# Optimization experiments

Measured on AMD Instinct MI355X. Metric: run time of the kernel, lower is better.

Reference implementation:

```python
import jax, jax.numpy as jnp
import numpy as np

HEADS = 16
NEG = -1.0e9


def setup_inputs() -> dict:
    key = jax.random.key(0)
    ks = jax.random.split(key, 6)
    B, T, E = 4, 2048, 1024
    s = 1.0 / np.sqrt(E)
    x = jax.random.normal(ks[0], (B, T, E), dtype=jnp.float32)
    Wq = jax.random.normal(ks[1], (E, E), dtype=jnp.float32) * s
    Wk = jax.random.normal(ks[2], (E, E), dtype=jnp.float32) * s
    Wv = jax.random.normal(ks[3], (E, E), dtype=jnp.float32) * s
    Wout = jax.random.normal(ks[4], (E, E), dtype=jnp.float32) * s
    bout = jax.random.normal(ks[5], (E,), dtype=jnp.float32) * 0.01
    return {"x": x, "Wq": Wq, "Wk": Wk, "Wv": Wv, "Wout": Wout, "bout": bout}


def reference(x, Wq, Wk, Wv, Wout, bout):
    B, T, E = x.shape
    H = HEADS
    D = E // H
    # nn.Linear(bias=False): y = x @ W.T
    Q = (x @ Wq.T).reshape(B, T, H, D).transpose(0, 2, 1, 3)  # [B,H,T,D]
    K = (x @ Wk.T).reshape(B, T, H, D).transpose(0, 2, 1, 3)
    V = (x @ Wv.T).reshape(B, T, H, D).transpose(0, 2, 1, 3)
    scores = jnp.einsum('bhqd,bhkd->bhqk', Q, K) / jnp.sqrt(jnp.float32(D))
    causal = jnp.tril(jnp.ones((T, T), dtype=bool))  # [T,T]
    scores = jnp.where(causal[None, None, :, :], scores, NEG)
    attn = jax.nn.softmax(scores, axis=-1)
    ctx = jnp.einsum('bhqk,bhkd->bhqd', attn, V)
    ctx = ctx.transpose(0, 2, 1, 3).reshape(B, T, E)
    return ctx @ Wout.T + bout
```

## Files before the change

### kernel.cpp

```cpp
#include <hip/hip_runtime.h>
#include <hip/hip_bf16.h>
#include <stdint.h>
#include <math.h>

#define B_ 4
#define T_ 2048
#define E_ 1024
#define H_ 16
#define D_ 64

typedef __attribute__((ext_vector_type(8))) short short8;
typedef __attribute__((ext_vector_type(4))) short short4v;
typedef __attribute__((ext_vector_type(4))) float f32x4;

#define MFMA_BF16(a, b, c) __builtin_amdgcn_mfma_f32_16x16x32_bf16((a), (b), (c), 0, 0, 0)

__device__ __forceinline__ unsigned short f2bf(float f) {
  union { float f; unsigned u; } v; v.f = f;
  unsigned r = v.u + 0x7FFFu + ((v.u >> 16) & 1u);
  return (unsigned short)(r >> 16);
}

#define GLOAD_LDS16(g, l)                                                        \
  __builtin_amdgcn_global_load_lds((const __attribute__((address_space(1))) void*)(g), \
                                   (__attribute__((address_space(3))) void*)(l), 16, 0, 0)

__global__ __launch_bounds__(256) void cvt_all(const float* __restrict__ x,
                                               const float* __restrict__ w0,
                                               const float* __restrict__ w1,
                                               const float* __restrict__ w2,
                                               const float* __restrict__ w3,
                                               unsigned short* __restrict__ xb,
                                               unsigned short* __restrict__ wb) {
  const int NX8 = 1048576;
  int i = blockIdx.x * blockDim.x + threadIdx.x;
  const float* src;
  unsigned short* dst;
  size_t off;
  if (i < NX8) {
    src = x; dst = xb; off = (size_t)i * 8;
  } else {
    int j = i - NX8;
    int which = j >> 17;
    int o = j & 131071;
    src = (which == 0) ? w0 : (which == 1) ? w1 : (which == 2) ? w2 : w3;
    dst = wb + ((size_t)which << 20);
    off = (size_t)o * 8;
  }
  const float4* p = (const float4*)(src + off);
  float4 a = p[0], b = p[1];
  short8 r;
  r[0] = (short)f2bf(a.x); r[1] = (short)f2bf(a.y);
  r[2] = (short)f2bf(a.z); r[3] = (short)f2bf(a.w);
  r[4] = (short)f2bf(b.x); r[5] = (short)f2bf(b.y);
  r[6] = (short)f2bf(b.z); r[7] = (short)f2bf(b.w);
  *(short8*)(dst + off) = r;
}


#define GEMM2_BODY(A_PTR, B_PTR)                                                  \
  const int K = E_;                                                               \
  const int NT = 16;                                                              \
  const int tid = threadIdx.x;                                                    \
  const int wid = tid >> 6;                                                       \
  const int lane = tid & 63;                                                      \
  const int lr = lane & 15;                                                       \
  const int lk = lane >> 4;                                                       \
  const int wm = wid >> 2, wn = wid & 3;                                          \
  const int srow = lane >> 3;                                                     \
  const int scol = ((lane & 7) ^ srow) * 8;                                       \
  const int rswz = (lr & 7) << 4;                                                 \
  const int kofs0 = (lk * 16) ^ rswz;                                             \
  const int kofs1 = (64 + lk * 16) ^ rswz;                                        \
  f32x4 acc[4][4] = {};                                                           \
  short8 af[4][2], bf0[2][2], bf1[2][2];                                          \
  auto stageA = [&](int tau) {                                                    \
    char* dst = lds + (tau & 1) * 49152 + wid * 1024;                             \
    const unsigned short* src = (A_PTR) + (size_t)(m0 + wid * 8 + srow) * K +     \
                                tau * 64 + scol;                                  \
    GLOAD_LDS16(src, dst);                                                        \
    GLOAD_LDS16(src + (size_t)64 * K, dst + 8192);                                \
  };                                                                              \
  auto stageB = [&](int tau) {                                                    \
    char* dst = lds + (tau & 1) * 49152 + 16384 + wid * 1024;                     \
    const unsigned short* src = (B_PTR) + (size_t)(n0 + wid * 8 + srow) * K +     \
                                tau * 64 + scol;                                  \
    GLOAD_LDS16(src, dst);                                                        \
    GLOAD_LDS16(src + (size_t)64 * K, dst + 8192);                                \
    GLOAD_LDS16(src + (size_t)128 * K, dst + 16384);                              \
    GLOAD_LDS16(src + (size_t)192 * K, dst + 24576);                              \
  };                                                                              \
  stageB(0); stageA(0); stageB(1);                                                \
  asm volatile("s_waitcnt vmcnt(4)" ::: "memory");                                \
  __builtin_amdgcn_s_barrier();                                                   \
  for (int t = 0; t < NT; ++t) {                                                  \
    char* bufA = lds + (t & 1) * 49152;                                           \
    char* bufB = bufA + 16384;                                                    \
    _Pragma("unroll")                                                             \
    for (int i = 0; i < 4; ++i) {                                                 \
      int row = wm * 64 + i * 16 + lr;                                            \
      af[i][0] = *(const short8*)(bufA + row * 128 + kofs0);                      \
      af[i][1] = *(const short8*)(bufA + row * 128 + kofs1);                      \
    }                                                                             \
    _Pragma("unroll")                                                             \
    for (int i = 0; i < 2; ++i) {                                                 \
      int row0 = wn * 64 + i * 16 + lr;                                           \
      int row1 = wn * 64 + (2 + i) * 16 + lr;                                     \
      bf0[i][0] = *(const short8*)(bufB + row0 * 128 + kofs0);                    \
      bf0[i][1] = *(const short8*)(bufB + row0 * 128 + kofs1);                    \
      bf1[i][0] = *(const short8*)(bufB + row1 * 128 + kofs0);                    \
      bf1[i][1] = *(const short8*)(bufB + row1 * 128 + kofs1);                    \
    }                                                                             \
    if (t + 1 < NT) stageA(t + 1);                                                \
    __builtin_amdgcn_s_barrier();                                                 \
    asm volatile("s_waitcnt lgkmcnt(0)" ::: "memory");                            \
    __builtin_amdgcn_sched_barrier(0);                                            \
    __builtin_amdgcn_s_setprio(1);                                                \
    _Pragma("unroll")                                                             \
    for (int i = 0; i < 4; ++i)                                                   \
      _Pragma("unroll")                                                           \
      for (int jn = 0; jn < 2; ++jn) {                                            \
        acc[i][jn] = MFMA_BF16(af[i][0], bf0[jn][0], acc[i][jn]);                 \
        acc[i][jn] = MFMA_BF16(af[i][1], bf0[jn][1], acc[i][jn]);                 \
      }                                                                           \
    __builtin_amdgcn_s_setprio(0);                                                \
    __builtin_amdgcn_s_barrier();                                                 \
    if (t + 2 < NT) stageB(t + 2);                                                \
    __builtin_amdgcn_s_setprio(1);                                                \
    _Pragma("unroll")                                                             \
    for (int i = 0; i < 4; ++i)                                                   \
      _Pragma("unroll")                                                           \
      for (int jn = 0; jn < 2; ++jn) {                                            \
        acc[i][2 + jn] = MFMA_BF16(af[i][0], bf1[jn][0], acc[i][2 + jn]);         \
        acc[i][2 + jn] = MFMA_BF16(af[i][1], bf1[jn][1], acc[i][2 + jn]);         \
      }                                                                           \
    __builtin_amdgcn_s_setprio(0);                                                \
    if (t < NT - 2) asm volatile("s_waitcnt vmcnt(4)" ::: "memory");              \
    else            asm volatile("s_waitcnt vmcnt(0)" ::: "memory");              \
    __builtin_amdgcn_s_barrier();                                                 \
  }

__global__ __launch_bounds__(512) void gemm_qkv2(const unsigned short* __restrict__ A,
                                                 const unsigned short* __restrict__ Wq,
                                                 const unsigned short* __restrict__ Wk,
                                                 const unsigned short* __restrict__ Wv,
                                                 unsigned short* __restrict__ Qo,
                                                 unsigned short* __restrict__ Ko,
                                                 unsigned short* __restrict__ Vo) {
  __shared__ __align__(16) char lds[98304];
  const int bid = blockIdx.x;
  const int xcd = bid & 7;
  const int p = bid >> 3;
  const int m0 = (xcd * 8 + (p & 7)) * 128;
  const int j = p >> 3;
  const int n0 = (j & 3) * 256;
  const int sel = j >> 2;
  const unsigned short* Bm = (sel == 0) ? Wq : (sel == 1) ? Wk : Wv;

  GEMM2_BODY(A, Bm)

  unsigned short* outp = (sel == 0) ? Qo : (sel == 1) ? Ko : Vo;
#pragma unroll
  for (int mi = 0; mi < 4; ++mi)
#pragma unroll
    for (int ni = 0; ni < 4; ++ni) {
      int row0 = m0 + wm * 64 + mi * 16 + lk * 4;
      int col = n0 + wn * 64 + ni * 16 + lr;
      int b = row0 >> 11, t0 = row0 & (T_ - 1), h = col >> 6, d = col & (D_ - 1);
      if (sel == 2) {
        short4v vv;
#pragma unroll
        for (int r = 0; r < 4; ++r) vv[r] = (short)f2bf(acc[mi][ni][r]);
        *(short4v*)&outp[(((size_t)(b * H_ + h)) * D_ + d) * T_ + t0] = vv;
      } else {
#pragma unroll
        for (int r = 0; r < 4; ++r)
          outp[(((size_t)(b * H_ + h)) * T_ + t0 + r) * D_ + d] = f2bf(acc[mi][ni][r]);
      }
    }
}

__global__ __launch_bounds__(512) void gemm_out2(const unsigned short* __restrict__ A,
                                                 const unsigned short* __restrict__ Wout,
                                                 float* __restrict__ outp,
                                                 const float* __restrict__ bias) {
  __shared__ __align__(16) char lds[98304];
  const int bid = blockIdx.x;
  const int xcd = bid & 7;
  const int p = bid >> 3;
  const int m0 = (xcd * 8 + (p & 7)) * 128;
  const int n0 = (p >> 3) * 256;

  GEMM2_BODY(A, Wout)

#pragma unroll
  for (int mi = 0; mi < 4; ++mi)
#pragma unroll
    for (int ni = 0; ni < 4; ++ni) {
      int row0 = m0 + wm * 64 + mi * 16 + lk * 4;
      int col = n0 + wn * 64 + ni * 16 + lr;
      float bv = bias[col];
#pragma unroll
      for (int r = 0; r < 4; ++r)
        outp[(size_t)(row0 + r) * E_ + col] = acc[mi][ni][r] + bv;
    }
}

__global__ __launch_bounds__(64) void attn_fused(const unsigned short* __restrict__ Q,
                                                 const unsigned short* __restrict__ K,
                                                 const unsigned short* __restrict__ VT,
                                                 unsigned short* __restrict__ ctx) {
  __shared__ __align__(16) unsigned short Pl[2][64 * 72];
  const int lane = threadIdx.x & 63;
  const int lr = lane & 15;
  const int lk = lane >> 4;

  const int bid = blockIdx.x;
  const int xcd = bid & 7;
  const int p = bid >> 3;
  const int bh = xcd * 8 + (p & 7);
  const int c = 31 - (p >> 3);
  const int q0 = c * 64;

  const unsigned short* Qh = Q + (size_t)bh * T_ * D_;
  const unsigned short* Kh = K + (size_t)bh * T_ * D_;
  const unsigned short* Vh = VT + (size_t)bh * T_ * D_;
  char* bufA = (char*)&Pl[0][0];
  char* bufB = (char*)&Pl[1][0];

  const float SC = 0.125f * 1.44269504089f;

  short8 vones;
#pragma unroll
  for (int j = 0; j < 8; ++j) vones[j] = (short)0x3F80;

  short8 qfA[2][2], qfB[2][2];
#pragma unroll
  for (int a = 0; a < 2; ++a)
#pragma unroll
    for (int kb = 0; kb < 2; ++kb) {
      qfA[a][kb] = *(const short8*)&Qh[(size_t)(q0 + a * 16 + lr) * D_ + kb * 32 + lk * 8];
      qfB[a][kb] = *(const short8*)&Qh[(size_t)(q0 + 32 + a * 16 + lr) * D_ + kb * 32 + lk * 8];
    }

  f32x4 oA[2][4] = {}, oB[2][4] = {};
  f32x4 lsA[2] = {}, lsB[2] = {};
  float mA[2] = {-1e30f, -1e30f}, mB[2] = {-1e30f, -1e30f};

  const int nt = c + 1;

  auto loadK = [&](short8(&kf)[2][4], int t) {
    const unsigned short* Kt = Kh + (size_t)t * 64 * D_;
#pragma unroll
    for (int kb = 0; kb < 2; ++kb)
#pragma unroll
      for (int n = 0; n < 4; ++n)
        kf[kb][n] = *(const short8*)&Kt[(size_t)(n * 16 + lr) * D_ + kb * 32 + lk * 8];
  };
  auto loadV = [&](short8(&v)[2][4], int t) {
    const unsigned short* Vtt = Vh + (size_t)t * 64;
#pragma unroll
    for (int kb = 0; kb < 2; ++kb)
#pragma unroll
      for (int nd = 0; nd < 4; ++nd)
        v[kb][nd] = *(const short8*)&Vtt[(size_t)(nd * 16 + lr) * T_ + kb * 32 + lk * 8];
  };
  auto rowmax = [&](f32x4(&st)[2][4], float(&pm)[2]) {
#pragma unroll
    for (int a = 0; a < 2; ++a) {
      float m0 = fmaxf(fmaxf(st[a][0][0], st[a][1][0]), fmaxf(st[a][2][0], st[a][3][0]));
      float m1 = fmaxf(fmaxf(st[a][0][1], st[a][1][1]), fmaxf(st[a][2][1], st[a][3][1]));
      float m2 = fmaxf(fmaxf(st[a][0][2], st[a][1][2]), fmaxf(st[a][2][2], st[a][3][2]));
      float m3 = fmaxf(fmaxf(st[a][0][3], st[a][1][3]), fmaxf(st[a][2][3], st[a][3][3]));
      float mx = fmaxf(fmaxf(m0, m1), fmaxf(m2, m3));
      mx = fmaxf(mx, __shfl_xor(mx, 16));
      mx = fmaxf(mx, __shfl_xor(mx, 32));
      pm[a] = mx * SC;
    }
  };
  auto rescale1 = [&](float(&pm)[2], float(&mrun)[2], f32x4(&ls)[2], f32x4(&o)[2][4]) {
#pragma unroll
    for (int a = 0; a < 2; ++a) {
      float mnew = fmaxf(mrun[a], pm[a]);
      float sc = exp2f(mrun[a] - mnew);
      mrun[a] = mnew;
#pragma unroll
      for (int r = 0; r < 4; ++r) {
        float sco = __shfl(sc, (lane & 48) | (lk * 4 + r));
        ls[a][r] *= sco;
#pragma unroll
        for (int nd = 0; nd < 4; ++nd) o[a][nd][r] *= sco;
      }
    }
  };
  auto pack = [&](f32x4(&st)[2][4], float(&mrun)[2], char* buf, int rb) {
#pragma unroll
    for (int a = 0; a < 2; ++a)
#pragma unroll
      for (int n = 0; n < 4; ++n) {
        float2 p01, p23;
        p01.x = exp2f(fmaf(st[a][n][0], SC, -mrun[a]));
        p01.y = exp2f(fmaf(st[a][n][1], SC, -mrun[a]));
        p23.x = exp2f(fmaf(st[a][n][2], SC, -mrun[a]));
        p23.y = exp2f(fmaf(st[a][n][3], SC, -mrun[a]));
        __hip_bfloat162 b01 = __float22bfloat162_rn(p01);
        __hip_bfloat162 b23 = __float22bfloat162_rn(p23);
        uint2 w;
        w.x = *(unsigned*)&b01;
        w.y = *(unsigned*)&b23;
        *(uint2*)(buf + (rb + a * 16 + lr) * 144 + n * 32 + lk * 8) = w;
      }
  };
  auto pv = [&](char* buf, short8(&v)[2][4]) {
#pragma unroll
    for (int kb = 0; kb < 2; ++kb) {
      short8 pfA0 = *(const short8*)(buf + (0 + lr) * 144 + kb * 64 + lk * 16);
      short8 pfA1 = *(const short8*)(buf + (16 + lr) * 144 + kb * 64 + lk * 16);
      short8 pfB0 = *(const short8*)(buf + (32 + lr) * 144 + kb * 64 + lk * 16);
      short8 pfB1 = *(const short8*)(buf + (48 + lr) * 144 + kb * 64 + lk * 16);
#pragma unroll
      for (int nd = 0; nd < 4; ++nd) {
        oA[0][nd] = MFMA_BF16(pfA0, v[kb][nd], oA[0][nd]);
        oA[1][nd] = MFMA_BF16(pfA1, v[kb][nd], oA[1][nd]);
        oB[0][nd] = MFMA_BF16(pfB0, v[kb][nd], oB[0][nd]);
        oB[1][nd] = MFMA_BF16(pfB1, v[kb][nd], oB[1][nd]);
      }
      lsA[0] = MFMA_BF16(pfA0, vones, lsA[0]);
      lsA[1] = MFMA_BF16(pfA1, vones, lsA[1]);
      lsB[0] = MFMA_BF16(pfB0, vones, lsB[0]);
      lsB[1] = MFMA_BF16(pfB1, vones, lsB[1]);
    }
  };

  auto tile = [&](int i, bool diag, bool doPV,
                  short8(&kfc)[2][4], short8(&kfn)[2][4],
                  short8(&vp)[2][4], short8(&vc)[2][4],
                  char* bufp, char* bufc, int tnext) {
    loadK(kfn, tnext);
    loadV(vc, i);
    f32x4 stA[2][4] = {}, stB[2][4] = {};
#pragma unroll
    for (int kb = 0; kb < 2; ++kb)
#pragma unroll
      for (int a = 0; a < 2; ++a)
#pragma unroll
        for (int n = 0; n < 4; ++n) {
          stA[a][n] = MFMA_BF16(kfc[kb][n], qfA[a][kb], stA[a][n]);
          stB[a][n] = MFMA_BF16(kfc[kb][n], qfB[a][kb], stB[a][n]);
        }
    if (diag) {
#pragma unroll
      for (int a = 0; a < 2; ++a)
#pragma unroll
        for (int n = 0; n < 4; ++n)
#pragma unroll
          for (int r = 0; r < 4; ++r) {
            if (n * 16 + lk * 4 + r > 0 + a * 16 + lr) stA[a][n][r] = -3e38f;
            if (n * 16 + lk * 4 + r > 32 + a * 16 + lr) stB[a][n][r] = -3e38f;
          }
    }
    float pmA[2], pmB[2];
    rowmax(stA, pmA);
    rowmax(stB, pmB);
    float need = fmaxf(fmaxf(pmA[0] - mA[0], pmA[1] - mA[1]),
                       fmaxf(pmB[0] - mB[0], pmB[1] - mB[1]));
    if (doPV) pv(bufp, vp);
    if (__any(need > 8.f)) {
      rescale1(pmA, mA, lsA, oA);
      rescale1(pmB, mB, lsB, oB);
    }
    pack(stA, mA, bufc, 0);
    pack(stB, mB, bufc, 32);
  };

  short8 kf0[2][4], kf1[2][4], v0[2][4], v1[2][4];

  loadK(kf0, 0);
  tile(0, nt == 1, false, kf0, kf1, v1, v0, bufB, bufA, (1 < nt) ? 1 : 0);

  int i = 1;
  while (i < nt) {
    tile(i, i == nt - 1, true, kf1, kf0, v0, v1, bufA, bufB, (i + 1 < nt) ? i + 1 : i);
    if (++i >= nt) break;
    tile(i, i == nt - 1, true, kf0, kf1, v1, v0, bufB, bufA, (i + 1 < nt) ? i + 1 : i);
    ++i;
  }
  if ((nt - 1) & 1) pv(bufB, v1);
  else              pv(bufA, v0);

  const int b = bh >> 4, h2 = bh & 15;
#pragma unroll
  for (int a = 0; a < 2; ++a)
#pragma unroll
    for (int r = 0; r < 4; ++r) {
      float invA = 1.0f / lsA[a][r];
      float invB = 1.0f / lsB[a][r];
      int tA = q0 + a * 16 + lk * 4 + r;
      int tB = tA + 32;
#pragma unroll
      for (int nd = 0; nd < 4; ++nd) {
        ctx[((size_t)b * T_ + tA) * E_ + h2 * D_ + nd * 16 + lr] = f2bf(oA[a][nd][r] * invA);
        ctx[((size_t)b * T_ + tB) * E_ + h2 * D_ + nd * 16 + lr] = f2bf(oB[a][nd][r] * invB);
      }
    }
}

extern "C" void kernel_launch(void* const* d_in, const int* in_sizes, int n_in,
                              void* d_out, int out_size, void* d_ws, size_t ws_size,
                              hipStream_t stream) {
  const float* x    = (const float*)d_in[0];
  const float* Wq   = (const float*)d_in[1];
  const float* Wk   = (const float*)d_in[2];
  const float* Wv   = (const float*)d_in[3];
  const float* Wout = (const float*)d_in[4];
  const float* bout = (const float*)d_in[5];
  float* out = (float*)d_out;

  const size_t MT = (size_t)B_ * T_;
  const size_t XE = MT * E_;
  const size_t WE = (size_t)E_ * E_;

  size_t need = (XE * 5 + WE * 4) * sizeof(unsigned short);
  if (ws_size < need) return;

  unsigned short* xb  = (unsigned short*)d_ws;
  unsigned short* wqb = xb + XE;
  unsigned short* wkb = wqb + WE;
  unsigned short* wvb = wkb + WE;
  unsigned short* wob = wvb + WE;
  unsigned short* Qb  = wob + WE;
  unsigned short* Kb  = Qb + XE;
  unsigned short* VTb = Kb + XE;
  unsigned short* ctx = VTb + XE;

  cvt_all<<<6144, 256, 0, stream>>>(x, Wq, Wk, Wv, Wout, xb, wqb);

  gemm_qkv2<<<768, 512, 0, stream>>>(xb, wqb, wkb, wvb, Qb, Kb, VTb);

  attn_fused<<<2048, 64, 0, stream>>>(Qb, Kb, VTb, ctx);

  gemm_out2<<<256, 512, 0, stream>>>(ctx, wob, out, bout);
}
```

Baseline: 167.2 us.

## Share K/V tiles via LDS across 8 waves per 256-row query block

The attention kernel changes from one 64-thread wave per 64-query chunk, which read K and V straight from global memory into registers, to 512-thread blocks. Each block covers 256 queries, with each wave owning 32 rows. K and V tiles are staged cooperatively into double-buffered, swizzled LDS with global_load_lds, so one copy serves all eight waves and global and L2 traffic drop. The cost is a block-wide barrier every tile, and waves whose causal range ends early sit idle while their siblings finish. The register-level software pipelining that overlapped PV with the next QK is also gone, and per-wave MFMA work per tile is halved.

Measured after the change: 169.2 us. No clear change (+1.2%).

```diff
diff --git a/kernel.cpp b/kernel.cpp
--- a/kernel.cpp
+++ b/kernel.cpp
@@ -56,7 +56,6 @@
   r[6] = (short)f2bf(b.z); r[7] = (short)f2bf(b.w);
   *(short8*)(dst + off) = r;
 }
-
 
 #define GEMM2_BODY(A_PTR, B_PTR)                                                  \
   const int K = E_;                                                               \
@@ -206,12 +205,15 @@
     }
 }
 
-__global__ __launch_bounds__(64) void attn_fused(const unsigned short* __restrict__ Q,
-                                                 const unsigned short* __restrict__ K,
-                                                 const unsigned short* __restrict__ VT,
-                                                 unsigned short* __restrict__ ctx) {
-  __shared__ __align__(16) unsigned short Pl[2][64 * 72];
-  const int lane = threadIdx.x & 63;
+__global__ __launch_bounds__(512) void attn_fused8(const unsigned short* __restrict__ Q,
+                                                   const unsigned short* __restrict__ K,
+                                                   const unsigned short* __restrict__ VT,
+                                                   unsigned short* __restrict__ ctx) {
+  __shared__ __align__(16) char kvb[2][16384];
+  __shared__ __align__(16) char Pl[8][4608];
+  const int tid = threadIdx.x;
+  const int wid = tid >> 6;
+  const int lane = tid & 63;
   const int lr = lane & 15;
   const int lk = lane >> 4;
 
@@ -219,189 +221,163 @@
   const int xcd = bid & 7;
   const int p = bid >> 3;
   const int bh = xcd * 8 + (p & 7);
-  const int c = 31 - (p >> 3);
-  const int q0 = c * 64;
+  const int Qb = 7 - (p >> 3);
 
   const unsigned short* Qh = Q + (size_t)bh * T_ * D_;
   const unsigned short* Kh = K + (size_t)bh * T_ * D_;
   const unsigned short* Vh = VT + (size_t)bh * T_ * D_;
-  char* bufA = (char*)&Pl[0][0];
-  char* bufB = (char*)&Pl[1][0];
+  char* Pb = Pl[wid];
+
+  const int q0w = Qb * 256 + wid * 32;
+  const int diag = q0w >> 6;
+  const int ql0 = (wid & 1) * 32;
+  const int NTb = 4 * Qb + 4;
 
   const float SC = 0.125f * 1.44269504089f;
 
+  const int srow = tid >> 3;
+  const int scol = ((tid & 7) ^ (srow & 7)) * 8;
+  const int rswz = (lr & 7) << 4;
+
+  auto stage = [&](int t) {
+    char* dst = kvb[t & 1] + tid * 16;
+    GLOAD_LDS16(Kh + (size_t)(t * 64 + srow) * D_ + scol, dst);
+    GLOAD_LDS16(Vh + (size_t)srow * T_ + t * 64 + scol, dst + 8192);
+  };
+
   short8 vones;
 #pragma unroll
   for (int j = 0; j < 8; ++j) vones[j] = (short)0x3F80;
 
-  short8 qfA[2][2], qfB[2][2];
+  short8 qf[2][2];
 #pragma unroll
   for (int a = 0; a < 2; ++a)
 #pragma unroll
-    for (int kb = 0; kb < 2; ++kb) {
-      qfA[a][kb] = *(const short8*)&Qh[(size_t)(q0 + a * 16 + lr) * D_ + kb * 32 + lk * 8];
-      qfB[a][kb] = *(const short8*)&Qh[(size_t)(q0 + 32 + a * 16 + lr) * D_ + kb * 32 + lk * 8];
-    }
-
-  f32x4 oA[2][4] = {}, oB[2][4] = {};
-  f32x4 lsA[2] = {}, lsB[2] = {};
-  float mA[2] = {-1e30f, -1e30f}, mB[2] = {-1e30f, -1e30f};
-
-  const int nt = c + 1;
-
-  auto loadK = [&](short8(&kf)[2][4], int t) {
-    const unsigned short* Kt = Kh + (size_t)t * 64 * D_;
-#pragma unroll
     for (int kb = 0; kb < 2; ++kb)
-#pragma unroll
-      for (int n = 0; n < 4; ++n)
-        kf[kb][n] = *(const short8*)&Kt[(size_t)(n * 16 + lr) * D_ + kb * 32 + lk * 8];
-  };
-  auto loadV = [&](short8(&v)[2][4], int t) {
-    const unsigned short* Vtt = Vh + (size_t)t * 64;
-#pragma unroll
-    for (int kb = 0; kb < 2; ++kb)
-#pragma unroll
-      for (int nd = 0; nd < 4; ++nd)
-        v[kb][nd] = *(const short8*)&Vtt[(size_t)(nd * 16 + lr) * T_ + kb * 32 + lk * 8];
-  };
-  auto rowmax = [&](f32x4(&st)[2][4], float(&pm)[2]) {
-#pragma unroll
-    for (int a = 0; a < 2; ++a) {
-      float m0 = fmaxf(fmaxf(st[a][0][0], st[a][1][0]), fmaxf(st[a][2][0], st[a][3][0]));
-      float m1 = fmaxf(fmaxf(st[a][0][1], st[a][1][1]), fmaxf(st[a][2][1], st[a][3][1]));
-      float m2 = fmaxf(fmaxf(st[a][0][2], st[a][1][2]), fmaxf(st[a][2][2], st[a][3][2]));
-      float m3 = fmaxf(fmaxf(st[a][0][3], st[a][1][3]), fmaxf(st[a][2][3], st[a][3][3]));
-      float mx = fmaxf(fmaxf(m0, m1), fmaxf(m2, m3));
-      mx = fmaxf(mx, __shfl_xor(mx, 16));
-      mx = fmaxf(mx, __shfl_xor(mx, 32));
-      pm[a] = mx * SC;
-    }
-  };
-  auto rescale1 = [&](float(&pm)[2], float(&mrun)[2], f32x4(&ls)[2], f32x4(&o)[2][4]) {
-#pragma unroll
-    for (int a = 0; a < 2; ++a) {
-      float mnew = fmaxf(mrun[a], pm[a]);
-      float sc = exp2f(mrun[a] - mnew);
-      mrun[a] = mnew;
-#pragma unroll
-      for (int r = 0; r < 4; ++r) {
-        float sco = __shfl(sc, (lane & 48) | (lk * 4 + r));
-        ls[a][r] *= sco;
-#pragma unroll
-        for (int nd = 0; nd < 4; ++nd) o[a][nd][r] *= sco;
+      qf[a][kb] = *(const short8*)&Qh[(size_t)(q0w + a * 16 + lr) * D_ + kb * 32 + lk * 8];
+
+  f32x4 o[2][4] = {};
+  f32x4 lsum[2] = {};
+  float mrun[2] = {-1e30f, -1e30f};
+
+  stage(0);
+  asm volatile("s_waitcnt vmcnt(0)" ::: "memory");
+  __builtin_amdgcn_s_barrier();
+
+  for (int t = 0; t < NTb; ++t) {
+    if (t + 1 < NTb) stage(t + 1);
+
+    if (t <= diag) {
+      char* kb_ = kvb[t & 1];
+      char* vb_ = kvb[t & 1] + 8192;
+
+      short8 kf[2][4];
+#pragma unroll
+      for (int kb = 0; kb < 2; ++kb)
+#pragma unroll
+        for (int n = 0; n < 4; ++n)
+          kf[kb][n] = *(const short8*)(kb_ + (n * 16 + lr) * 128 + ((kb * 64 + lk * 16) ^ rswz));
+
+      f32x4 st[2][4] = {};
+#pragma unroll
+      for (int kb = 0; kb < 2; ++kb)
+#pragma unroll
+        for (int a = 0; a < 2; ++a)
+#pragma unroll
+          for (int n = 0; n < 4; ++n)
+            st[a][n] = MFMA_BF16(kf[kb][n], qf[a][kb], st[a][n]);
+
+      if (t == diag) {
+#pragma unroll
+        for (int a = 0; a < 2; ++a)
+#pragma unroll
+          for (int n = 0; n < 4; ++n)
+#pragma unroll
+            for (int r = 0; r < 4; ++r)
+              if (n * 16 + lk * 4 + r > ql0 + a * 16 + lr) st[a][n][r] = -3e38f;
+      }
+
+      float pm[2];
+#pragma unroll
+      for (int a = 0; a < 2; ++a) {
+        float m0 = fmaxf(fmaxf(st[a][0][0], st[a][1][0]), fmaxf(st[a][2][0], st[a][3][0]));
+        float m1 = fmaxf(fmaxf(st[a][0][1], st[a][1][1]), fmaxf(st[a][2][1], st[a][3][1]));
+        float m2 = fmaxf(fmaxf(st[a][0][2], st[a][1][2]), fmaxf(st[a][2][2], st[a][3][2]));
+        float m3 = fmaxf(fmaxf(st[a][0][3], st[a][1][3]), fmaxf(st[a][2][3], st[a][3][3]));
+        float mx = fmaxf(fmaxf(m0, m1), fmaxf(m2, m3));
+        mx = fmaxf(mx, __shfl_xor(mx, 16));
+        mx = fmaxf(mx, __shfl_xor(mx, 32));
+        pm[a] = mx * SC;
+      }
+      float need = fmaxf(pm[0] - mrun[0], pm[1] - mrun[1]);
+
+      if (__any(need > 8.f)) {
+#pragma unroll
+        for (int a = 0; a < 2; ++a) {
+          float mnew = fmaxf(mrun[a], pm[a]);
+          float sc = exp2f(mrun[a] - mnew);
+          mrun[a] = mnew;
+#pragma unroll
+          for (int r = 0; r < 4; ++r) {
+            float sco = __shfl(sc, (lane & 48) | (lk * 4 + r));
+            lsum[a][r] *= sco;
+#pragma unroll
+            for (int nd = 0; nd < 4; ++nd) o[a][nd][r] *= sco;
+          }
+        }
+      }
+
+#pragma unroll
+      for (int a = 0; a < 2; ++a)
+#pragma unroll
+        for (int n = 0; n < 4; ++n) {
+          float2 p01, p23;
+          p01.x = exp2f(fmaf(st[a][n][0], SC, -mrun[a]));
+          p01.y = exp2f(fmaf(st[a][n][1], SC, -mrun[a]));
+          p23.x = exp2f(fmaf(st[a][n][2], SC, -mrun[a]));
+          p23.y = exp2f(fmaf(st[a][n][3], SC, -mrun[a]));
+          __hip_bfloat162 b01 = __float22bfloat162_rn(p01);
+          __hip_bfloat162 b23 = __float22bfloat162_rn(p23);
+          uint2 w;
+          w.x = *(unsigned*)&b01;
+          w.y = *(unsigned*)&b23;
+          *(uint2*)(Pb + (a * 16 + lr) * 144 + n * 32 + lk * 8) = w;
+        }
+
+      short8 vf[2][4];
+#pragma unroll
+      for (int kb = 0; kb < 2; ++kb)
+#pragma unroll
+        for (int nd = 0; nd < 4; ++nd)
+          vf[kb][nd] = *(const short8*)(vb_ + (nd * 16 + lr) * 128 + ((kb * 64 + lk * 16) ^ rswz));
+#pragma unroll
+      for (int kb = 0; kb < 2; ++kb) {
+        short8 pf0 = *(const short8*)(Pb + (0 + lr) * 144 + kb * 64 + lk * 16);
+        short8 pf1 = *(const short8*)(Pb + (16 + lr) * 144 + kb * 64 + lk * 16);
+#pragma unroll
+        for (int nd = 0; nd < 4; ++nd) {
+          o[0][nd] = MFMA_BF16(pf0, vf[kb][nd], o[0][nd]);
+          o[1][nd] = MFMA_BF16(pf1, vf[kb][nd], o[1][nd]);
+        }
+        lsum[0] = MFMA_BF16(pf0, vones, lsum[0]);
+        lsum[1] = MFMA_BF16(pf1, vones, lsum[1]);
       }
     }
-  };
-  auto pack = [&](f32x4(&st)[2][4], float(&mrun)[2], char* buf, int rb) {
-#pragma unroll
-    for (int a = 0; a < 2; ++a)
-#pragma unroll
-      for (int n = 0; n < 4; ++n) {
-        float2 p01, p23;
-        p01.x = exp2f(fmaf(st[a][n][0], SC, -mrun[a]));
-        p01.y = exp2f(fmaf(st[a][n][1], SC, -mrun[a]));
-        p23.x = exp2f(fmaf(st[a][n][2], SC, -mrun[a]));
-        p23.y = exp2f(fmaf(st[a][n][3], SC, -mrun[a]));
-        __hip_bfloat162 b01 = __float22bfloat162_rn(p01);
-        __hip_bfloat162 b23 = __float22bfloat162_rn(p23);
-        uint2 w;
-        w.x = *(unsigned*)&b01;
-        w.y = *(unsigned*)&b23;
-        *(uint2*)(buf + (rb + a * 16 + lr) * 144 + n * 32 + lk * 8) = w;
-      }
-  };
-  auto pv = [&](char* buf, short8(&v)[2][4]) {
-#pragma unroll
-    for (int kb = 0; kb < 2; ++kb) {
-      short8 pfA0 = *(const short8*)(buf + (0 + lr) * 144 + kb * 64 + lk * 16);
-      short8 pfA1 = *(const short8*)(buf + (16 + lr) * 144 + kb * 64 + lk * 16);
-      short8 pfB0 = *(const short8*)(buf + (32 + lr) * 144 + kb * 64 + lk * 16);
-      short8 pfB1 = *(const short8*)(buf + (48 + lr) * 144 + kb * 64 + lk * 16);
-#pragma unroll
-      for (int nd = 0; nd < 4; ++nd) {
-        oA[0][nd] = MFMA_BF16(pfA0, v[kb][nd], oA[0][nd]);
-        oA[1][nd] = MFMA_BF16(pfA1, v[kb][nd], oA[1][nd]);
-        oB[0][nd] = MFMA_BF16(pfB0, v[kb][nd], oB[0][nd]);
-        oB[1][nd] = MFMA_BF16(pfB1, v[kb][nd], oB[1][nd]);
-      }
-      lsA[0] = MFMA_BF16(pfA0, vones, lsA[0]);
-      lsA[1] = MFMA_BF16(pfA1, vones, lsA[1]);
-      lsB[0] = MFMA_BF16(pfB0, vones, lsB[0]);
-      lsB[1] = MFMA_BF16(pfB1, vones, lsB[1]);
-    }
-  };
-
-  auto tile = [&](int i, bool diag, bool doPV,
-                  short8(&kfc)[2][4], short8(&kfn)[2][4],
-                  short8(&vp)[2][4], short8(&vc)[2][4],
-                  char* bufp, char* bufc, int tnext) {
-    loadK(kfn, tnext);
-    loadV(vc, i);
-    f32x4 stA[2][4] = {}, stB[2][4] = {};
-#pragma unroll
-    for (int kb = 0; kb < 2; ++kb)
-#pragma unroll
-      for (int a = 0; a < 2; ++a)
-#pragma unroll
-        for (int n = 0; n < 4; ++n) {
-          stA[a][n] = MFMA_BF16(kfc[kb][n], qfA[a][kb], stA[a][n]);
-          stB[a][n] = MFMA_BF16(kfc[kb][n], qfB[a][kb], stB[a][n]);
-        }
-    if (diag) {
-#pragma unroll
-      for (int a = 0; a < 2; ++a)
-#pragma unroll
-        for (int n = 0; n < 4; ++n)
-#pragma unroll
-          for (int r = 0; r < 4; ++r) {
-            if (n * 16 + lk * 4 + r > 0 + a * 16 + lr) stA[a][n][r] = -3e38f;
-            if (n * 16 + lk * 4 + r > 32 + a * 16 + lr) stB[a][n][r] = -3e38f;
-          }
-    }
-    float pmA[2], pmB[2];
-    rowmax(stA, pmA);
-    rowmax(stB, pmB);
-    float need = fmaxf(fmaxf(pmA[0] - mA[0], pmA[1] - mA[1]),
-                       fmaxf(pmB[0] - mB[0], pmB[1] - mB[1]));
-    if (doPV) pv(bufp, vp);
-    if (__any(need > 8.f)) {
-      rescale1(pmA, mA, lsA, oA);
-      rescale1(pmB, mB, lsB, oB);
-    }
-    pack(stA, mA, bufc, 0);
-    pack(stB, mB, bufc, 32);
-  };
-
-  short8 kf0[2][4], kf1[2][4], v0[2][4], v1[2][4];
-
-  loadK(kf0, 0);
-  tile(0, nt == 1, false, kf0, kf1, v1, v0, bufB, bufA, (1 < nt) ? 1 : 0);
-
-  int i = 1;
-  while (i < nt) {
-    tile(i, i == nt - 1, true, kf1, kf0, v0, v1, bufA, bufB, (i + 1 < nt) ? i + 1 : i);
-    if (++i >= nt) break;
-    tile(i, i == nt - 1, true, kf0, kf1, v1, v0, bufB, bufA, (i + 1 < nt) ? i + 1 : i);
-    ++i;
+
+    asm volatile("s_waitcnt vmcnt(0)" ::: "memory");
+    __builtin_amdgcn_s_barrier();
   }
-  if ((nt - 1) & 1) pv(bufB, v1);
-  else              pv(bufA, v0);
 
   const int b = bh >> 4, h2 = bh & 15;
 #pragma unroll
   for (int a = 0; a < 2; ++a)
 #pragma unroll
     for (int r = 0; r < 4; ++r) {
-      float invA = 1.0f / lsA[a][r];
-      float invB = 1.0f / lsB[a][r];
-      int tA = q0 + a * 16 + lk * 4 + r;
-      int tB = tA + 32;
-#pragma unroll
-      for (int nd = 0; nd < 4; ++nd) {
-        ctx[((size_t)b * T_ + tA) * E_ + h2 * D_ + nd * 16 + lr] = f2bf(oA[a][nd][r] * invA);
-        ctx[((size_t)b * T_ + tB) * E_ + h2 * D_ + nd * 16 + lr] = f2bf(oB[a][nd][r] * invB);
-      }
+      float inv = 1.0f / lsum[a][r];
+      int tq = q0w + a * 16 + lk * 4 + r;
+#pragma unroll
+      for (int nd = 0; nd < 4; ++nd)
+        ctx[((size_t)b * T_ + tq) * E_ + h2 * D_ + nd * 16 + lr] = f2bf(o[a][nd][r] * inv);
     }
 }
 
@@ -437,7 +413,7 @@
 
   gemm_qkv2<<<768, 512, 0, stream>>>(xb, wqb, wkb, wvb, Qb, Kb, VTb);
 
-  attn_fused<<<2048, 64, 0, stream>>>(Qb, Kb, VTb, ctx);
+  attn_fused8<<<512, 512, 0, stream>>>(Qb, Kb, VTb, ctx);
 
   gemm_out2<<<256, 512, 0, stream>>>(ctx, wob, out, bout);
 }
```
